# Performance work log

Measured on AMD Instinct MI355X. Metric: run time of the kernel, lower is better.

The kernel has to match this reference:

```python
import jax, jax.numpy as jnp
import numpy as np

B, T, D, H = 4, 2048, 384, 6
HD = D // H  # 64
HALF = HD // 2


def setup_inputs() -> dict:
    key = jax.random.key(0)
    k0, k1, k2 = jax.random.split(key, 3)
    x = jax.random.normal(k0, (B, T, D), jnp.float32)
    attn_bias = jnp.zeros((1, 1, T, T), jnp.float32)  # additive SDPA bias
    # standard RoPE tables: [T, HD/2]
    inv_freq = 1.0 / (10000.0 ** (np.arange(HALF, dtype=np.float32) / HALF))
    ang = np.arange(T, dtype=np.float32)[:, None] * inv_freq[None, :]
    cos = jnp.asarray(np.cos(ang), jnp.float32)
    sin = jnp.asarray(np.sin(ang), jnp.float32)
    w_qkv = jax.random.normal(k1, (D, 3 * D), jnp.float32) * (D ** -0.5)
    w_proj = jax.random.normal(k2, (D, D), jnp.float32) * (D ** -0.5)
    return {"x": x, "attn_bias": attn_bias, "cos": cos, "sin": sin,
            "w_qkv": w_qkv, "w_proj": w_proj}


def _apply_rope(x, cos, sin):
    # x: [b, h, t, hd]; cos/sin: [t, hd/2] -> rotate-half RoPE
    half = x.shape[-1] // 2
    x1, x2 = x[..., :half], x[..., half:]
    c = cos[None, None, :, :]
    s = sin[None, None, :, :]
    return jnp.concatenate([x1 * c - x2 * s, x2 * c + x1 * s], axis=-1)


def reference(x, attn_bias, cos, sin, w_qkv, w_proj):
    b, t, _ = x.shape
    qkv = (x @ w_qkv).reshape(b, t, 3, H, HD)  # fused QKV projection
    q = jnp.transpose(qkv[:, :, 0], (0, 2, 1, 3))  # [b,h,t,hd]
    k = jnp.transpose(qkv[:, :, 1], (0, 2, 1, 3))
    v = jnp.transpose(qkv[:, :, 2], (0, 2, 1, 3))
    q = _apply_rope(q, cos, sin)
    k = _apply_rope(k, cos, sin)
    scale = 1.0 / jnp.sqrt(jnp.asarray(HD, x.dtype))
    scores = jnp.einsum("bhqd,bhkd->bhqk", q, k) * scale + attn_bias
    attn = jax.nn.softmax(scores, axis=-1)
    out = jnp.einsum("bhqk,bhkd->bhqd", attn, v)
    out = jnp.transpose(out, (0, 2, 1, 3)).reshape(b, t, H * HD)
    return out @ w_proj
```

## Files before the change

kernel.cpp:

```cpp
#include <hip/hip_runtime.h>
#include <hip/hip_bf16.h>

#define BB   4
#define TT   2048
#define DDIM 384
#define HH   6
#define HD   64
#define BT   (BB*TT)
#define QKVC (3*DDIM)

typedef __attribute__((ext_vector_type(4))) short short4v;
typedef __attribute__((ext_vector_type(8))) short short8v;
typedef __attribute__((ext_vector_type(4))) float float4v;
typedef unsigned short u16;

static __device__ __forceinline__ u16 f2bu(float f) {
    __hip_bfloat16 h = __float2bfloat16(f);
    return __builtin_bit_cast(u16, h);
}

static __device__ __forceinline__ short8v ld_frag(const u16* p) {
    short4v a = *(const short4v*)p;
    short4v b = *(const short4v*)(p + 4);
    return __builtin_shufflevector(a, b, 0, 1, 2, 3, 4, 5, 6, 7);
}

static __device__ __forceinline__ void st8(u16* p, uint4 v) {
    *(uint2*)p       = make_uint2(v.x, v.y);
    *(uint2*)(p + 4) = make_uint2(v.z, v.w);
}

#define MFMA16(a, b, c) __builtin_amdgcn_mfma_f32_16x16x32_bf16((a), (b), (c), 0, 0, 0)

__global__ __launch_bounds__(256) void wtrans_kernel(
    const float* __restrict__ in, u16* __restrict__ out, int K, int C)
{
    __shared__ float tr[64][65];
    const int t = threadIdx.x;
    const int c0 = blockIdx.x * 64, k0 = blockIdx.y * 64;
    {
        int kr = t >> 2, cb = (t & 3) * 16;
        const float* gp = in + (size_t)(k0 + kr) * C + c0 + cb;
        #pragma unroll
        for (int u = 0; u < 4; ++u) {
            float4 v = *(const float4*)(gp + 4 * u);
            tr[cb + 4 * u + 0][kr] = v.x;
            tr[cb + 4 * u + 1][kr] = v.y;
            tr[cb + 4 * u + 2][kr] = v.z;
            tr[cb + 4 * u + 3][kr] = v.w;
        }
    }
    __syncthreads();
    {
        int c = t >> 2, kb = (t & 3) * 16;
        __align__(16) u16 tmp[16];
        #pragma unroll
        for (int u = 0; u < 16; ++u) tmp[u] = f2bu(tr[c][kb + u]);
        u16* op = out + (size_t)(c0 + c) * K + k0 + kb;
        *(short8v*)op       = *(const short8v*)tmp;
        *(short8v*)(op + 8) = *(const short8v*)(tmp + 8);
    }
}

__global__ __launch_bounds__(256) void qkv_rope_kernel(
    const float* __restrict__ x, const u16* __restrict__ wt,
    const float* __restrict__ cs, const float* __restrict__ sn,
    u16* __restrict__ qb, u16* __restrict__ kb, u16* __restrict__ vtb)
{
    __shared__ __align__(16) u16 xs[2][64][68];
    __shared__ __align__(16) u16 ws[2][64][68];
    const int t = threadIdx.x;
    const int wv = t >> 6, lane = t & 63, quad = lane >> 4, lo = lane & 15;
    const int r0 = blockIdx.y * 64;
    const int c0 = blockIdx.x * 64;

    const int xr = t >> 2, xk = (t & 3) * 16;
    const int wc = t >> 3, wk = (t & 7) * 8;

    {
        const float* gp = x + (size_t)(r0 + xr) * DDIM + xk;
        #pragma unroll
        for (int u = 0; u < 4; ++u) {
            float4 v = *(const float4*)(gp + 4 * u);
            unsigned a0 = f2bu(v.x) | ((unsigned)f2bu(v.y) << 16);
            unsigned a1 = f2bu(v.z) | ((unsigned)f2bu(v.w) << 16);
            *(uint2*)&xs[0][xr][xk + 4 * u] = make_uint2(a0, a1);
        }
        st8(&ws[0][wc][wk],      *(const uint4*)(wt + (size_t)(c0 + wc) * DDIM + wk));
        st8(&ws[0][wc + 32][wk], *(const uint4*)(wt + (size_t)(c0 + wc + 32) * DDIM + wk));
    }
    __syncthreads();

    float4v acc[4] = {};
    for (int kk = 0; kk < 6; ++kk) {
        const int cur = kk & 1, nxt = cur ^ 1;
        const int kkn = (kk < 5 ? kk + 1 : 5) * 64;
        float4 xp[4];
        const float* gp = x + (size_t)(r0 + xr) * DDIM + kkn + xk;
        #pragma unroll
        for (int u = 0; u < 4; ++u) xp[u] = *(const float4*)(gp + 4 * u);
        uint4 wp0 = *(const uint4*)(wt + (size_t)(c0 + wc) * DDIM + kkn + wk);
        uint4 wp1 = *(const uint4*)(wt + (size_t)(c0 + wc + 32) * DDIM + kkn + wk);

        #pragma unroll
        for (int kf = 0; kf < 2; ++kf) {
            short8v a = ld_frag(&xs[cur][16 * wv + lo][kf * 32 + quad * 8]);
            #pragma unroll
            for (int nt = 0; nt < 4; ++nt) {
                short8v b = ld_frag(&ws[cur][nt * 16 + lo][kf * 32 + quad * 8]);
                acc[nt] = MFMA16(a, b, acc[nt]);
            }
        }
        #pragma unroll
        for (int u = 0; u < 4; ++u) {
            unsigned a0 = f2bu(xp[u].x) | ((unsigned)f2bu(xp[u].y) << 16);
            unsigned a1 = f2bu(xp[u].z) | ((unsigned)f2bu(xp[u].w) << 16);
            *(uint2*)&xs[nxt][xr][xk + 4 * u] = make_uint2(a0, a1);
        }
        st8(&ws[nxt][wc][wk], wp0);
        st8(&ws[nxt][wc + 32][wk], wp1);
        __syncthreads();
    }

    const int sec = blockIdx.x / 6;
    const int h   = blockIdx.x % 6;
    const int rbase = r0 + 16 * wv + 4 * quad;
    const int bidx  = r0 >> 11;
    const int tbase = rbase & (TT - 1);

    if (sec == 2) {
        #pragma unroll
        for (int nt = 0; nt < 4; ++nt) {
            int d = nt * 16 + lo;
            unsigned a0 = f2bu(acc[nt][0]) | ((unsigned)f2bu(acc[nt][1]) << 16);
            unsigned a1 = f2bu(acc[nt][2]) | ((unsigned)f2bu(acc[nt][3]) << 16);
            u16* gp = vtb + ((size_t)(bidx * HH + h) * HD + d) * TT + tbase;
            *(uint2*)gp = make_uint2(a0, a1);
        }
    } else {
        u16* dst = (sec == 0) ? qb : kb;
        #pragma unroll
        for (int np = 0; np < 2; ++np) {
            #pragma unroll
            for (int r = 0; r < 4; ++r) {
                int tpos = tbase + r;
                int ci = np * 16 + lo;
                float cv = cs[tpos * 32 + ci];
                float sv = sn[tpos * 32 + ci];
                float x1 = acc[np][r], x2 = acc[np + 2][r];
                u16* gp = dst + ((size_t)(bidx * HH + h) * TT + tpos) * HD;
                gp[ci]      = f2bu(x1 * cv - x2 * sv);
                gp[ci + 32] = f2bu(x2 * cv + x1 * sv);
            }
        }
    }
}

__global__ __launch_bounds__(256, 3) void attn_kernel(
    const u16* __restrict__ qb, const u16* __restrict__ kb, const u16* __restrict__ vtb,
    const float* __restrict__ bias, u16* __restrict__ ob)
{
    __shared__ __align__(16) u16 ks[2][64][68];
    __shared__ __align__(16) u16 vt[2][64][68];
    __shared__ __align__(16) u16 ps[4][16][68];

    const int t = threadIdx.x;
    const int wv = t >> 6, lane = t & 63, quad = lane >> 4, lo = lane & 15;
    const int bh = blockIdx.y;
    const int b = bh / HH, h = bh % HH;
    const int q0 = blockIdx.x * 64;
    const int qrow = q0 + 16 * wv + 4 * quad;

    const u16* qbase = qb + ((size_t)bh * TT + q0 + 16 * wv + lo) * HD + quad * 8;
    short8v aq[2];
    aq[0] = __builtin_bit_cast(short8v, *(const uint4*)qbase);
    aq[1] = __builtin_bit_cast(short8v, *(const uint4*)(qbase + 32));

    const int sr = t >> 3, sd = (t & 7) * 8;
    const u16* kbbase = kb + (size_t)bh * TT * HD;
    const u16* vtbase = vtb + (size_t)bh * HD * TT;

    st8(&ks[0][sr][sd],      *(const uint4*)(kbbase + (size_t)sr * HD + sd));
    st8(&ks[0][sr + 32][sd], *(const uint4*)(kbbase + (size_t)(sr + 32) * HD + sd));
    st8(&vt[0][sr][sd],      *(const uint4*)(vtbase + (size_t)sr * TT + sd));
    st8(&vt[0][sr + 32][sd], *(const uint4*)(vtbase + (size_t)(sr + 32) * TT + sd));
    float bcur[4][4];
    #pragma unroll
    for (int nt = 0; nt < 4; ++nt)
        #pragma unroll
        for (int r = 0; r < 4; ++r)
            bcur[nt][r] = bias[(size_t)(qrow + r) * TT + nt * 16 + lo];
    __syncthreads();

    float4v oacc[4] = {};
    float lacc[4] = {0.f, 0.f, 0.f, 0.f};

    for (int kt = 0; kt < TT / 64; ++kt) {
        const int cur = kt & 1, nxt = cur ^ 1;
        const int kn = (kt < 31 ? kt + 1 : 31) * 64;

        uint4 kp0 = *(const uint4*)(kbbase + (size_t)(kn + sr) * HD + sd);
        uint4 kp1 = *(const uint4*)(kbbase + (size_t)(kn + sr + 32) * HD + sd);
        uint4 vp0 = *(const uint4*)(vtbase + (size_t)sr * TT + kn + sd);
        uint4 vp1 = *(const uint4*)(vtbase + (size_t)(sr + 32) * TT + kn + sd);
        float bnxt[4][4];
        #pragma unroll
        for (int nt = 0; nt < 4; ++nt)
            #pragma unroll
            for (int r = 0; r < 4; ++r)
                bnxt[nt][r] = bias[(size_t)(qrow + r) * TT + kn + nt * 16 + lo];

        float4v s[4] = {};
        #pragma unroll
        for (int kf = 0; kf < 2; ++kf) {
            #pragma unroll
            for (int nt = 0; nt < 4; ++nt) {
                short8v bfr = ld_frag(&ks[cur][nt * 16 + lo][kf * 32 + quad * 8]);
                s[nt] = MFMA16(aq[kf], bfr, s[nt]);
            }
        }

        #pragma unroll
        for (int nt = 0; nt < 4; ++nt)
            #pragma unroll
            for (int r = 0; r < 4; ++r) {
                float p = __expf(s[nt][r] * 0.125f + bcur[nt][r]);
                lacc[r] += p;
                ps[wv][4 * quad + r][nt * 16 + lo] = f2bu(p);
            }

        #pragma unroll
        for (int kf = 0; kf < 2; ++kf) {
            short8v ap = ld_frag(&ps[wv][lo][kf * 32 + quad * 8]);
            #pragma unroll
            for (int nt = 0; nt < 4; ++nt) {
                short8v bv = ld_frag(&vt[cur][nt * 16 + lo][kf * 32 + quad * 8]);
                oacc[nt] = MFMA16(ap, bv, oacc[nt]);
            }
        }

        st8(&ks[nxt][sr][sd], kp0);
        st8(&ks[nxt][sr + 32][sd], kp1);
        st8(&vt[nxt][sr][sd], vp0);
        st8(&vt[nxt][sr + 32][sd], vp1);
        #pragma unroll
        for (int nt = 0; nt < 4; ++nt)
            #pragma unroll
            for (int r = 0; r < 4; ++r)
                bcur[nt][r] = bnxt[nt][r];
        __syncthreads();
    }

    #pragma unroll
    for (int r = 0; r < 4; ++r) {
        float l = lacc[r];
        l += __shfl_xor(l, 1);
        l += __shfl_xor(l, 2);
        l += __shfl_xor(l, 4);
        l += __shfl_xor(l, 8);
        float inv = 1.f / l;
        u16* gp = ob + ((size_t)b * TT + qrow + r) * DDIM + h * HD;
        #pragma unroll
        for (int nt = 0; nt < 4; ++nt)
            gp[nt * 16 + lo] = f2bu(oacc[nt][r] * inv);
    }
}

__global__ __launch_bounds__(256) void proj_kernel(
    const u16* __restrict__ o, const u16* __restrict__ wt, float* __restrict__ out)
{
    __shared__ __align__(16) u16 os[2][64][68];
    __shared__ __align__(16) u16 ws[2][64][68];
    const int t = threadIdx.x;
    const int wv = t >> 6, lane = t & 63, quad = lane >> 4, lo = lane & 15;
    const int r0 = blockIdx.y * 64, c0 = blockIdx.x * 64;
    const int sr = t >> 3, sd = (t & 7) * 8;

    st8(&os[0][sr][sd],      *(const uint4*)(o + (size_t)(r0 + sr) * DDIM + sd));
    st8(&os[0][sr + 32][sd], *(const uint4*)(o + (size_t)(r0 + sr + 32) * DDIM + sd));
    st8(&ws[0][sr][sd],      *(const uint4*)(wt + (size_t)(c0 + sr) * DDIM + sd));
    st8(&ws[0][sr + 32][sd], *(const uint4*)(wt + (size_t)(c0 + sr + 32) * DDIM + sd));
    __syncthreads();

    float4v acc[4] = {};
    for (int kk = 0; kk < 6; ++kk) {
        const int cur = kk & 1, nxt = cur ^ 1;
        const int kkn = (kk < 5 ? kk + 1 : 5) * 64;
        uint4 op0 = *(const uint4*)(o + (size_t)(r0 + sr) * DDIM + kkn + sd);
        uint4 op1 = *(const uint4*)(o + (size_t)(r0 + sr + 32) * DDIM + kkn + sd);
        uint4 wp0 = *(const uint4*)(wt + (size_t)(c0 + sr) * DDIM + kkn + sd);
        uint4 wp1 = *(const uint4*)(wt + (size_t)(c0 + sr + 32) * DDIM + kkn + sd);

        #pragma unroll
        for (int kf = 0; kf < 2; ++kf) {
            short8v a = ld_frag(&os[cur][16 * wv + lo][kf * 32 + quad * 8]);
            #pragma unroll
            for (int nt = 0; nt < 4; ++nt) {
                short8v bfr = ld_frag(&ws[cur][nt * 16 + lo][kf * 32 + quad * 8]);
                acc[nt] = MFMA16(a, bfr, acc[nt]);
            }
        }
        st8(&os[nxt][sr][sd], op0);
        st8(&os[nxt][sr + 32][sd], op1);
        st8(&ws[nxt][sr][sd], wp0);
        st8(&ws[nxt][sr + 32][sd], wp1);
        __syncthreads();
    }
    #pragma unroll
    for (int r = 0; r < 4; ++r) {
        float* gp = out + (size_t)(r0 + 16 * wv + 4 * quad + r) * DDIM + c0;
        #pragma unroll
        for (int nt = 0; nt < 4; ++nt)
            gp[nt * 16 + lo] = acc[nt][r];
    }
}

extern "C" void kernel_launch(void* const* d_in, const int* in_sizes, int n_in,
                              void* d_out, int out_size, void* d_ws, size_t ws_size,
                              hipStream_t stream) {
    const float* x     = (const float*)d_in[0];
    const float* bias  = (const float*)d_in[1];
    const float* cs    = (const float*)d_in[2];
    const float* sn    = (const float*)d_in[3];
    const float* wqkv  = (const float*)d_in[4];
    const float* wproj = (const float*)d_in[5];
    float* out = (float*)d_out;

    u16* wqkvT  = (u16*)d_ws;
    u16* wprojT = wqkvT + (size_t)QKVC * DDIM;
    u16* qb     = wprojT + (size_t)DDIM * DDIM;
    u16* kb     = qb + (size_t)BB * HH * TT * HD;
    u16* vtb    = kb + (size_t)BB * HH * TT * HD;
    u16* ob     = vtb + (size_t)BB * HH * TT * HD;

    wtrans_kernel<<<dim3(QKVC / 64, DDIM / 64), 256, 0, stream>>>(wqkv, wqkvT, DDIM, QKVC);
    wtrans_kernel<<<dim3(DDIM / 64, DDIM / 64), 256, 0, stream>>>(wproj, wprojT, DDIM, DDIM);
    qkv_rope_kernel<<<dim3(QKVC / 64, BT / 64), 256, 0, stream>>>(x, wqkvT, cs, sn, qb, kb, vtb);
    attn_kernel<<<dim3(TT / 64, BB * HH), 256, 0, stream>>>(qb, kb, vtb, bias, ob);
    proj_kernel<<<dim3(DDIM / 64, BT / 64), 256, 0, stream>>>(ob, wprojT, out);
}
```

Measured before the change: 180.9 us.

## Keep P in registers via transposed S, pre-convert x to bf16, merge prep kernels

The attention kernel now computes S transposed (K as the A operand) so each lane holds probabilities along the key dimension. These feed a 16x16x16 MFMA for P·V directly from registers, which removes the shared-memory round trip for P. Bias loads become float4 vector loads. The two weight-transpose launches and a new x-to-bf16 conversion are merged into one prep kernel, so the QKV GEMM loads pre-converted bf16 x instead of converting fp32 in every column tile; this costs an extra global write and read of x in bf16. The change also risks twice as many smaller MFMAs in the P·V step.

Measured after the change: 191.3 us. 1.06x slower.

```diff
diff --git a/kernel.cpp b/kernel.cpp
--- a/kernel.cpp
+++ b/kernel.cpp
@@ -32,12 +32,41 @@
 
 #define MFMA16(a, b, c) __builtin_amdgcn_mfma_f32_16x16x32_bf16((a), (b), (c), 0, 0, 0)
 
-__global__ __launch_bounds__(256) void wtrans_kernel(
-    const float* __restrict__ in, u16* __restrict__ out, int K, int C)
+#if __has_builtin(__builtin_amdgcn_mfma_f32_16x16x16_bf16)
+#define MFMAK16(a, b, c) __builtin_amdgcn_mfma_f32_16x16x16_bf16((a), (b), (c), 0, 0, 0)
+#elif __has_builtin(__builtin_amdgcn_mfma_f32_16x16x16bf16_1k)
+#define MFMAK16(a, b, c) __builtin_amdgcn_mfma_f32_16x16x16bf16_1k((a), (b), (c), 0, 0, 0)
+#else
+#define MFMAK16(a, b, c) __builtin_amdgcn_mfma_f32_16x16x16bf16_1k((a), (b), (c), 0, 0, 0)
+#endif
+
+__global__ __launch_bounds__(256) void prep_kernel(
+    const float* __restrict__ wqkv, const float* __restrict__ wproj,
+    const float* __restrict__ x,
+    u16* __restrict__ wqkvT, u16* __restrict__ wprojT, u16* __restrict__ xb)
 {
+    const int bid = blockIdx.x;
+    const int t = threadIdx.x;
+    if (bid >= 144) {
+        size_t base = (size_t)(bid - 144) * 4096 + (size_t)t * 16;
+        const float* gp = x + base;
+        __align__(16) u16 tmp[16];
+        #pragma unroll
+        for (int u = 0; u < 4; ++u) {
+            float4 v = *(const float4*)(gp + 4 * u);
+            tmp[4 * u + 0] = f2bu(v.x); tmp[4 * u + 1] = f2bu(v.y);
+            tmp[4 * u + 2] = f2bu(v.z); tmp[4 * u + 3] = f2bu(v.w);
+        }
+        *(uint4*)(xb + base)     = *(const uint4*)tmp;
+        *(uint4*)(xb + base + 8) = *(const uint4*)(tmp + 8);
+        return;
+    }
+    const float* in; u16* out; int K, C, c0, k0;
+    if (bid < 108) { in = wqkv;  out = wqkvT;  K = DDIM; C = QKVC;
+                     c0 = (bid % 18) * 64; k0 = (bid / 18) * 64; }
+    else           { int b2 = bid - 108; in = wproj; out = wprojT; K = DDIM; C = DDIM;
+                     c0 = (b2 % 6) * 64; k0 = (b2 / 6) * 64; }
     __shared__ float tr[64][65];
-    const int t = threadIdx.x;
-    const int c0 = blockIdx.x * 64, k0 = blockIdx.y * 64;
     {
         int kr = t >> 2, cb = (t & 3) * 16;
         const float* gp = in + (size_t)(k0 + kr) * C + c0 + cb;
@@ -57,13 +86,13 @@
         #pragma unroll
         for (int u = 0; u < 16; ++u) tmp[u] = f2bu(tr[c][kb + u]);
         u16* op = out + (size_t)(c0 + c) * K + k0 + kb;
-        *(short8v*)op       = *(const short8v*)tmp;
-        *(short8v*)(op + 8) = *(const short8v*)(tmp + 8);
+        *(uint4*)op       = *(const uint4*)tmp;
+        *(uint4*)(op + 8) = *(const uint4*)(tmp + 8);
     }
 }
 
 __global__ __launch_bounds__(256) void qkv_rope_kernel(
-    const float* __restrict__ x, const u16* __restrict__ wt,
+    const u16* __restrict__ xb, const u16* __restrict__ wt,
     const float* __restrict__ cs, const float* __restrict__ sn,
     u16* __restrict__ qb, u16* __restrict__ kb, u16* __restrict__ vtb)
 {
@@ -73,34 +102,22 @@
     const int wv = t >> 6, lane = t & 63, quad = lane >> 4, lo = lane & 15;
     const int r0 = blockIdx.y * 64;
     const int c0 = blockIdx.x * 64;
-
-    const int xr = t >> 2, xk = (t & 3) * 16;
-    const int wc = t >> 3, wk = (t & 7) * 8;
-
-    {
-        const float* gp = x + (size_t)(r0 + xr) * DDIM + xk;
-        #pragma unroll
-        for (int u = 0; u < 4; ++u) {
-            float4 v = *(const float4*)(gp + 4 * u);
-            unsigned a0 = f2bu(v.x) | ((unsigned)f2bu(v.y) << 16);
-            unsigned a1 = f2bu(v.z) | ((unsigned)f2bu(v.w) << 16);
-            *(uint2*)&xs[0][xr][xk + 4 * u] = make_uint2(a0, a1);
-        }
-        st8(&ws[0][wc][wk],      *(const uint4*)(wt + (size_t)(c0 + wc) * DDIM + wk));
-        st8(&ws[0][wc + 32][wk], *(const uint4*)(wt + (size_t)(c0 + wc + 32) * DDIM + wk));
-    }
+    const int sr = t >> 3, sd = (t & 7) * 8;
+
+    st8(&xs[0][sr][sd],      *(const uint4*)(xb + (size_t)(r0 + sr) * DDIM + sd));
+    st8(&xs[0][sr + 32][sd], *(const uint4*)(xb + (size_t)(r0 + sr + 32) * DDIM + sd));
+    st8(&ws[0][sr][sd],      *(const uint4*)(wt + (size_t)(c0 + sr) * DDIM + sd));
+    st8(&ws[0][sr + 32][sd], *(const uint4*)(wt + (size_t)(c0 + sr + 32) * DDIM + sd));
     __syncthreads();
 
     float4v acc[4] = {};
     for (int kk = 0; kk < 6; ++kk) {
         const int cur = kk & 1, nxt = cur ^ 1;
         const int kkn = (kk < 5 ? kk + 1 : 5) * 64;
-        float4 xp[4];
-        const float* gp = x + (size_t)(r0 + xr) * DDIM + kkn + xk;
-        #pragma unroll
-        for (int u = 0; u < 4; ++u) xp[u] = *(const float4*)(gp + 4 * u);
-        uint4 wp0 = *(const uint4*)(wt + (size_t)(c0 + wc) * DDIM + kkn + wk);
-        uint4 wp1 = *(const uint4*)(wt + (size_t)(c0 + wc + 32) * DDIM + kkn + wk);
+        uint4 xp0 = *(const uint4*)(xb + (size_t)(r0 + sr) * DDIM + kkn + sd);
+        uint4 xp1 = *(const uint4*)(xb + (size_t)(r0 + sr + 32) * DDIM + kkn + sd);
+        uint4 wp0 = *(const uint4*)(wt + (size_t)(c0 + sr) * DDIM + kkn + sd);
+        uint4 wp1 = *(const uint4*)(wt + (size_t)(c0 + sr + 32) * DDIM + kkn + sd);
 
         #pragma unroll
         for (int kf = 0; kf < 2; ++kf) {
@@ -111,14 +128,10 @@
                 acc[nt] = MFMA16(a, b, acc[nt]);
             }
         }
-        #pragma unroll
-        for (int u = 0; u < 4; ++u) {
-            unsigned a0 = f2bu(xp[u].x) | ((unsigned)f2bu(xp[u].y) << 16);
-            unsigned a1 = f2bu(xp[u].z) | ((unsigned)f2bu(xp[u].w) << 16);
-            *(uint2*)&xs[nxt][xr][xk + 4 * u] = make_uint2(a0, a1);
-        }
-        st8(&ws[nxt][wc][wk], wp0);
-        st8(&ws[nxt][wc + 32][wk], wp1);
+        st8(&xs[nxt][sr][sd], xp0);
+        st8(&xs[nxt][sr + 32][sd], xp1);
+        st8(&ws[nxt][sr][sd], wp0);
+        st8(&ws[nxt][sr + 32][sd], wp1);
         __syncthreads();
     }
 
@@ -162,34 +175,30 @@
 {
     __shared__ __align__(16) u16 ks[2][64][68];
     __shared__ __align__(16) u16 vt[2][64][68];
-    __shared__ __align__(16) u16 ps[4][16][68];
 
     const int t = threadIdx.x;
     const int wv = t >> 6, lane = t & 63, quad = lane >> 4, lo = lane & 15;
     const int bh = blockIdx.y;
     const int b = bh / HH, h = bh % HH;
     const int q0 = blockIdx.x * 64;
-    const int qrow = q0 + 16 * wv + 4 * quad;
-
-    const u16* qbase = qb + ((size_t)bh * TT + q0 + 16 * wv + lo) * HD + quad * 8;
-    short8v aq[2];
-    aq[0] = __builtin_bit_cast(short8v, *(const uint4*)qbase);
-    aq[1] = __builtin_bit_cast(short8v, *(const uint4*)(qbase + 32));
+    const int qrow = q0 + 16 * wv + lo;
+
+    const u16* qbase = qb + ((size_t)bh * TT + qrow) * HD + quad * 8;
+    short8v aq0 = __builtin_bit_cast(short8v, *(const uint4*)qbase);
+    short8v aq1 = __builtin_bit_cast(short8v, *(const uint4*)(qbase + 32));
 
     const int sr = t >> 3, sd = (t & 7) * 8;
     const u16* kbbase = kb + (size_t)bh * TT * HD;
     const u16* vtbase = vtb + (size_t)bh * HD * TT;
+    const float* brow = bias + (size_t)qrow * TT + 4 * quad;
 
     st8(&ks[0][sr][sd],      *(const uint4*)(kbbase + (size_t)sr * HD + sd));
     st8(&ks[0][sr + 32][sd], *(const uint4*)(kbbase + (size_t)(sr + 32) * HD + sd));
     st8(&vt[0][sr][sd],      *(const uint4*)(vtbase + (size_t)sr * TT + sd));
     st8(&vt[0][sr + 32][sd], *(const uint4*)(vtbase + (size_t)(sr + 32) * TT + sd));
-    float bcur[4][4];
+    float4 bcur[4];
     #pragma unroll
-    for (int nt = 0; nt < 4; ++nt)
-        #pragma unroll
-        for (int r = 0; r < 4; ++r)
-            bcur[nt][r] = bias[(size_t)(qrow + r) * TT + nt * 16 + lo];
+    for (int nt = 0; nt < 4; ++nt) bcur[nt] = *(const float4*)(brow + nt * 16);
     __syncthreads();
 
     float4v oacc[4] = {};
@@ -203,39 +212,39 @@
         uint4 kp1 = *(const uint4*)(kbbase + (size_t)(kn + sr + 32) * HD + sd);
         uint4 vp0 = *(const uint4*)(vtbase + (size_t)sr * TT + kn + sd);
         uint4 vp1 = *(const uint4*)(vtbase + (size_t)(sr + 32) * TT + kn + sd);
-        float bnxt[4][4];
-        #pragma unroll
-        for (int nt = 0; nt < 4; ++nt)
-            #pragma unroll
-            for (int r = 0; r < 4; ++r)
-                bnxt[nt][r] = bias[(size_t)(qrow + r) * TT + kn + nt * 16 + lo];
+        float4 bnxt[4];
+        #pragma unroll
+        for (int nt = 0; nt < 4; ++nt) bnxt[nt] = *(const float4*)(brow + kn + nt * 16);
 
         float4v s[4] = {};
         #pragma unroll
         for (int kf = 0; kf < 2; ++kf) {
             #pragma unroll
             for (int nt = 0; nt < 4; ++nt) {
-                short8v bfr = ld_frag(&ks[cur][nt * 16 + lo][kf * 32 + quad * 8]);
-                s[nt] = MFMA16(aq[kf], bfr, s[nt]);
-            }
-        }
-
-        #pragma unroll
-        for (int nt = 0; nt < 4; ++nt)
-            #pragma unroll
-            for (int r = 0; r < 4; ++r) {
-                float p = __expf(s[nt][r] * 0.125f + bcur[nt][r]);
-                lacc[r] += p;
-                ps[wv][4 * quad + r][nt * 16 + lo] = f2bu(p);
-            }
-
-        #pragma unroll
-        for (int kf = 0; kf < 2; ++kf) {
-            short8v ap = ld_frag(&ps[wv][lo][kf * 32 + quad * 8]);
+                short8v kfr = ld_frag(&ks[cur][nt * 16 + lo][kf * 32 + quad * 8]);
+                s[nt] = MFMA16(kfr, (kf ? aq1 : aq0), s[nt]);
+            }
+        }
+
+        short4v pa[4];
+        #pragma unroll
+        for (int nt = 0; nt < 4; ++nt) {
+            float p0 = __expf(fmaf(s[nt][0], 0.125f, bcur[nt].x));
+            float p1 = __expf(fmaf(s[nt][1], 0.125f, bcur[nt].y));
+            float p2 = __expf(fmaf(s[nt][2], 0.125f, bcur[nt].z));
+            float p3 = __expf(fmaf(s[nt][3], 0.125f, bcur[nt].w));
+            lacc[nt] += (p0 + p1) + (p2 + p3);
+            short4v pv = { (short)f2bu(p0), (short)f2bu(p1),
+                           (short)f2bu(p2), (short)f2bu(p3) };
+            pa[nt] = pv;
+        }
+
+        #pragma unroll
+        for (int dt = 0; dt < 4; ++dt) {
             #pragma unroll
             for (int nt = 0; nt < 4; ++nt) {
-                short8v bv = ld_frag(&vt[cur][nt * 16 + lo][kf * 32 + quad * 8]);
-                oacc[nt] = MFMA16(ap, bv, oacc[nt]);
+                short4v bv = *(const short4v*)&vt[cur][dt * 16 + lo][nt * 16 + 4 * quad];
+                oacc[dt] = MFMAK16(pa[nt], bv, oacc[dt]);
             }
         }
 
@@ -244,25 +253,21 @@
         st8(&vt[nxt][sr][sd], vp0);
         st8(&vt[nxt][sr + 32][sd], vp1);
         #pragma unroll
-        for (int nt = 0; nt < 4; ++nt)
-            #pragma unroll
-            for (int r = 0; r < 4; ++r)
-                bcur[nt][r] = bnxt[nt][r];
+        for (int nt = 0; nt < 4; ++nt) bcur[nt] = bnxt[nt];
         __syncthreads();
     }
 
+    float l = (lacc[0] + lacc[1]) + (lacc[2] + lacc[3]);
+    l += __shfl_xor(l, 16);
+    l += __shfl_xor(l, 32);
     #pragma unroll
     for (int r = 0; r < 4; ++r) {
-        float l = lacc[r];
-        l += __shfl_xor(l, 1);
-        l += __shfl_xor(l, 2);
-        l += __shfl_xor(l, 4);
-        l += __shfl_xor(l, 8);
-        float inv = 1.f / l;
-        u16* gp = ob + ((size_t)b * TT + qrow + r) * DDIM + h * HD;
-        #pragma unroll
-        for (int nt = 0; nt < 4; ++nt)
-            gp[nt * 16 + lo] = f2bu(oacc[nt][r] * inv);
+        float lr = __shfl(l, 4 * quad + r);
+        float inv = 1.f / lr;
+        u16* gp = ob + ((size_t)b * TT + q0 + 16 * wv + 4 * quad + r) * DDIM + h * HD + lo;
+        #pragma unroll
+        for (int dt = 0; dt < 4; ++dt)
+            gp[dt * 16] = f2bu(oacc[dt][r] * inv);
     }
 }
 
@@ -332,10 +337,12 @@
     u16* kb     = qb + (size_t)BB * HH * TT * HD;
     u16* vtb    = kb + (size_t)BB * HH * TT * HD;
     u16* ob     = vtb + (size_t)BB * HH * TT * HD;
-
-    wtrans_kernel<<<dim3(QKVC / 64, DDIM / 64), 256, 0, stream>>>(wqkv, wqkvT, DDIM, QKVC);
-    wtrans_kernel<<<dim3(DDIM / 64, DDIM / 64), 256, 0, stream>>>(wproj, wprojT, DDIM, DDIM);
-    qkv_rope_kernel<<<dim3(QKVC / 64, BT / 64), 256, 0, stream>>>(x, wqkvT, cs, sn, qb, kb, vtb);
+    u16* xb     = ob + (size_t)BT * DDIM;
+
+    prep_kernel<<<dim3(144 + BT * DDIM / 4096), 256, 0, stream>>>(
+        wqkv, wproj, x, wqkvT, wprojT, xb);
+    qkv_rope_kernel<<<dim3(QKVC / 64, BT / 64), 256, 0, stream>>>(
+        xb, wqkvT, cs, sn, qb, kb, vtb);
     attn_kernel<<<dim3(TT / 64, BB * HH), 256, 0, stream>>>(qb, kb, vtb, bias, ob);
     proj_kernel<<<dim3(DDIM / 64, BT / 64), 256, 0, stream>>>(ob, wprojT, out);
 }
```
